# Optimization experiments

Hardware: AMD Instinct MI355X
Metric: run time of the kernel (lower is better)

Reference implementation:

```python
import jax, jax.numpy as jnp
import numpy as np

B, Q, H = 1, 1024, 2048
NH, NKV, HD = 32, 8, 64
KB = 2048
THETA = 10000.0
KB_MAX_TRAIN = 4096.0


def _bitlinear(x, w):
    """BitNet b1.58 linear: per-token int8 absmax activation quant + ternary weight quant (STE)."""
    a_scale = 127.0 / jnp.clip(jnp.max(jnp.abs(x), axis=-1, keepdims=True), 1e-5)
    xq = jnp.clip(jnp.round(x * a_scale), -128.0, 127.0) / a_scale
    w_scale = 1.0 / jnp.clip(jnp.mean(jnp.abs(w)), 1e-5)
    wq = jnp.clip(jnp.round(w * w_scale), -1.0, 1.0) / w_scale
    x_ste = x + jax.lax.stop_gradient(xq - x)
    w_ste = w + jax.lax.stop_gradient(wq - w)
    return jnp.einsum('bsh,oh->bso', x_ste, w_ste)


def _rope_cos_sin(position_ids):
    inv_freq = 1.0 / (THETA ** (jnp.arange(0, HD, 2, dtype=jnp.float32) / HD))  # [HD/2]
    freqs = position_ids.astype(jnp.float32)[..., None] * inv_freq  # [B,Q,HD/2]
    emb = jnp.concatenate([freqs, freqs], axis=-1)  # [B,Q,HD]
    return jnp.cos(emb)[:, None], jnp.sin(emb)[:, None]  # [B,1,Q,HD]


def _rotate_half(x):
    return jnp.concatenate([-x[..., HD // 2:], x[..., :HD // 2]], axis=-1)


def setup_inputs() -> dict:
    key = jax.random.key(0)
    ks = jax.random.split(key, 9)
    hidden_states = jax.random.normal(ks[0], (B, Q, H), jnp.float32)
    # additive causal mask
    attention_mask = jnp.triu(jnp.full((Q, Q), -1e9, jnp.float32), 1)[None, None]
    kb_keys = jax.random.normal(ks[1], (B, NH, KB, HD), jnp.float32)
    kb_values = jax.random.normal(ks[2], (B, NH, KB, HD), jnp.float32)
    s = 0.02
    Wq = jax.random.normal(ks[3], (NH * HD, H), jnp.float32) * s
    Wk = jax.random.normal(ks[4], (NKV * HD, H), jnp.float32) * s
    Wv = jax.random.normal(ks[5], (NKV * HD, H), jnp.float32) * s
    Wo = jax.random.normal(ks[6], (H, NH * HD), jnp.float32) * s
    Wq_new = jax.random.normal(ks[7], (NH * HD, H), jnp.float32) * s
    position_ids = jnp.arange(Q, dtype=jnp.int32)[None, :]
    return dict(hidden_states=hidden_states, attention_mask=attention_mask,
                kb_keys=kb_keys, kb_values=kb_values,
                Wq=Wq, Wk=Wk, Wv=Wv, Wo=Wo, Wq_new=Wq_new,
                position_ids=position_ids)


def reference(hidden_states, attention_mask, kb_keys, kb_values,
              Wq, Wk, Wv, Wo, Wq_new, position_ids):
    b, q_len, _ = hidden_states.shape
    # BitLinear QKV projections
    q = _bitlinear(hidden_states, Wq).reshape(b, q_len, NH, HD).transpose(0, 2, 1, 3)
    k = _bitlinear(hidden_states, Wk).reshape(b, q_len, NKV, HD).transpose(0, 2, 1, 3)
    v = _bitlinear(hidden_states, Wv).reshape(b, q_len, NKV, HD).transpose(0, 2, 1, 3)
    # RoPE on prompt q/k (KB query is NOT rotated, matching the source)
    cos, sin = _rope_cos_sin(position_ids)
    q = q * cos + _rotate_half(q) * sin
    k = k * cos + _rotate_half(k) * sin
    # GQA: repeat kv heads
    groups = NH // NKV
    k = jnp.repeat(k, groups, axis=1)
    v = jnp.repeat(v, groups, axis=1)
    # KB query via separate BitLinear
    kb_q = _bitlinear(hidden_states, Wq_new).reshape(b, q_len, NH, HD).transpose(0, 2, 1, 3)
    scale = 1.0 / jnp.sqrt(jnp.float32(HD))
    kb_len = kb_keys.shape[2]
    scores_kb = jnp.einsum('bhqd,bhkd->bhqk', kb_q, kb_keys) * scale
    scores_kb = scores_kb + (jnp.log(jnp.float32(KB_MAX_TRAIN)) - jnp.log(jnp.float32(kb_len)))
    scores_p = jnp.einsum('bhqd,bhkd->bhqk', q, k) * scale + attention_mask
    attn = jax.nn.softmax(jnp.concatenate([scores_kb, scores_p], axis=-1).astype(jnp.float32), axis=-1)
    out = (jnp.einsum('bhqk,bhkd->bhqd', attn[..., :kb_len], kb_values)
           + jnp.einsum('bhqk,bhkd->bhqd', attn[..., kb_len:], v))
    out = out.transpose(0, 2, 1, 3).reshape(b, q_len, NH * HD)
    return _bitlinear(out, Wo)
```

## Files before the change

kernel.cpp:

```cpp
#include <hip/hip_runtime.h>
#include <hip/hip_bf16.h>
#include <stdint.h>
#include <math.h>

#define cH    2048
#define cQ    1024
#define cNH   32
#define cNKV  8
#define cKB   2048

#define INV_BIG   (1.0f/4194304.0f)
#define INV_SMALL (1.0f/1048576.0f)

#define WS_SUMS 0
#define WS_DQ1  256
#define WS_DQ2  4352
#define WS_XQ   8448
#define WS_WALL 4202752
#define WS_QB   25174272
#define WS_KB   33562880
#define WS_VB   35660032
#define WS_QN   37757184
#define WS_ROPET 46145792


using short8  = __attribute__((ext_vector_type(8))) short;
using floatx4 = __attribute__((ext_vector_type(4))) float;

__device__ __forceinline__ void bsplit(float x, unsigned short& hi, unsigned short& lo) {
  __hip_bfloat16 h = __float2bfloat16(x);
  float hf = __bfloat162float(h);
  __hip_bfloat16 l = __float2bfloat16(x - hf);
  hi = *(unsigned short*)&h;
  lo = *(unsigned short*)&l;
}

__device__ __forceinline__ unsigned short tern(float v, float ws) {
  float q = rintf(v * ws);
  q = fminf(fmaxf(q, -1.0f), 1.0f);
  return (unsigned short)(__float_as_uint(q) >> 16);
}

__device__ __forceinline__ void gload16(const void* g, void* l) {
  __builtin_amdgcn_global_load_lds((const __attribute__((address_space(1))) void*)g,
                                   (__attribute__((address_space(3))) void*)l, 16, 0, 0);
}

__global__ void k_ropetab(const int* __restrict__ pos, float2* __restrict__ tab) {
  int i = blockIdx.x * 256 + threadIdx.x;
  int t = i >> 5, d = i & 31;
  double p = (double)pos[t];
  double ang = p * pow(10000.0, -(double)d / 32.0);
  tab[i] = make_float2((float)cos(ang), (float)sin(ang));
}

__global__ void k_abssum5(const float* __restrict__ w0, const float* __restrict__ w1,
                          const float* __restrict__ w2, const float* __restrict__ w3,
                          const float* __restrict__ w4, double* __restrict__ out) {
  __shared__ double red[256];
  const int seg = blockIdx.y;
  const float* w = seg == 0 ? w0 : seg == 1 ? w1 : seg == 2 ? w2 : seg == 3 ? w3 : w4;
  const int n4 = ((seg == 1 || seg == 2) ? 512 * 2048 : 2048 * 2048) / 4;
  double s = 0.0;
  for (int i = blockIdx.x * 256 + threadIdx.x; i < n4; i += gridDim.x * 256) {
    float4 x = *(const float4*)(w + (size_t)i * 4);
    s += (double)fabsf(x.x) + (double)fabsf(x.y) + (double)fabsf(x.z) + (double)fabsf(x.w);
  }
  red[threadIdx.x] = s;
  __syncthreads();
  for (int o = 128; o > 0; o >>= 1) {
    if ((int)threadIdx.x < o) red[threadIdx.x] += red[threadIdx.x + o];
    __syncthreads();
  }
  if (threadIdx.x == 0) atomicAdd(out + seg, red[0]);
}

__global__ void k_wquant4(const float* __restrict__ Wq, const float* __restrict__ Wk,
                          const float* __restrict__ Wv, const float* __restrict__ Wqn,
                          unsigned short* __restrict__ wall, const double* __restrict__ sums) {
  size_t i = ((size_t)blockIdx.x * 256 + threadIdx.x) * 4;
  const float* src; size_t off; double s; float inv;
  if (i < 4194304)      { src = Wq;  off = 0;       s = sums[0]; inv = INV_BIG; }
  else if (i < 5242880) { src = Wk;  off = 4194304; s = sums[1]; inv = INV_SMALL; }
  else if (i < 6291456) { src = Wv;  off = 5242880; s = sums[2]; inv = INV_SMALL; }
  else                  { src = Wqn; off = 6291456; s = sums[4]; inv = INV_BIG; }
  float ws = 1.0f / fmaxf((float)s * inv, 1e-5f);
  float4 x = *(const float4*)(src + (i - off));
  ushort4 o;
  o.x = tern(x.x, ws); o.y = tern(x.y, ws); o.z = tern(x.z, ws); o.w = tern(x.w, ws);
  *(ushort4*)(wall + i) = o;
}

__global__ void k_wquant(const float* __restrict__ w, unsigned short* __restrict__ wq,
                         const double* __restrict__ sum, float inv_n) {
  size_t i = ((size_t)blockIdx.x * 256 + threadIdx.x) * 4;
  float ws = 1.0f / fmaxf((float)(*sum) * inv_n, 1e-5f);
  float4 x = *(const float4*)(w + i);
  ushort4 o;
  o.x = tern(x.x, ws); o.y = tern(x.y, ws); o.z = tern(x.z, ws); o.w = tern(x.w, ws);
  *(ushort4*)(wq + i) = o;
}

__global__ void k_aquant(const float* __restrict__ x, unsigned short* __restrict__ xq,
                         float* __restrict__ dq, int K) {
  int t = blockIdx.x;
  const float4* xr = (const float4*)(x + (size_t)t * K);
  const int K4 = K / 4;
  __shared__ float red[256];
  float m = 0.0f;
  for (int i = threadIdx.x; i < K4; i += 256) {
    float4 v = xr[i];
    m = fmaxf(m, fmaxf(fmaxf(fabsf(v.x), fabsf(v.y)), fmaxf(fabsf(v.z), fabsf(v.w))));
  }
  red[threadIdx.x] = m;
  __syncthreads();
  for (int o = 128; o > 0; o >>= 1) {
    if ((int)threadIdx.x < o) red[threadIdx.x] = fmaxf(red[threadIdx.x], red[threadIdx.x + o]);
    __syncthreads();
  }
  float amax = fmaxf(red[0], 1e-5f);
  float as = 127.0f / amax;
  ushort4* xo = (ushort4*)(xq + (size_t)t * K);
  for (int i = threadIdx.x; i < K4; i += 256) {
    float4 v = xr[i];
    ushort4 o;
    float q;
    q = fminf(fmaxf(rintf(v.x * as), -128.0f), 127.0f); o.x = (unsigned short)(__float_as_uint(q) >> 16);
    q = fminf(fmaxf(rintf(v.y * as), -128.0f), 127.0f); o.y = (unsigned short)(__float_as_uint(q) >> 16);
    q = fminf(fmaxf(rintf(v.z * as), -128.0f), 127.0f); o.z = (unsigned short)(__float_as_uint(q) >> 16);
    q = fminf(fmaxf(rintf(v.w * as), -128.0f), 127.0f); o.w = (unsigned short)(__float_as_uint(q) >> 16);
    xo[i] = o;
  }
  if (threadIdx.x == 0) dq[t] = amax / 127.0f;
}

__global__ __launch_bounds__(256) void k_gemm_mfma(
    const unsigned short* __restrict__ Aq, const unsigned short* __restrict__ Ball,
    const float* __restrict__ adq, const double* __restrict__ sums,
    const float2* __restrict__ ropetab,
    float* __restrict__ oQ, unsigned short* __restrict__ oKhi,
    unsigned short* __restrict__ oKlo,
    float* __restrict__ oV, float* __restrict__ oQN, int mode) {
  __shared__ __attribute__((aligned(16))) unsigned short As[2][128 * 64];
  __shared__ __attribute__((aligned(16))) unsigned short Bs[2][128 * 64];
  const int t = threadIdx.x;
  const int lane = t & 63;
  const int row16 = lane & 15, q = lane >> 4;
  const int w = t >> 6;
  const int wm = (w >> 1) * 64, wn = (w & 1) * 64;
  const int bx = blockIdx.x;
  const int m0 = blockIdx.y * 128;
  const unsigned short* Bp = Ball + (size_t)bx * 128 * 2048;
  const int swr = row16 & 7;

  floatx4 acc[4][4];
#pragma unroll
  for (int g = 0; g < 4; ++g)
#pragma unroll
    for (int h = 0; h < 4; ++h) acc[g][h] = (floatx4){0.f, 0.f, 0.f, 0.f};

  auto stageAB = [&](int k0s, int b) {
#pragma unroll
    for (int i = 0; i < 4; ++i) {
      int c = t + 256 * i;
      int row = c >> 3, g8 = c & 7;
      int sa = (g8 ^ (row & 7)) * 8;
      gload16(Aq + (size_t)(m0 + row) * 2048 + k0s + sa, &As[b][w * 512 + i * 2048]);
      gload16(Bp + (size_t)row * 2048 + k0s + sa, &Bs[b][w * 512 + i * 2048]);
    }
  };

  stageAB(0, 0);
  for (int k0 = 0; k0 < 2048; k0 += 64) {
    const int cur = (k0 >> 6) & 1;
    const int kn = (k0 + 64 < 2048) ? k0 + 64 : k0;
    stageAB(kn, cur ^ 1);
    asm volatile("s_waitcnt vmcnt(8)" ::: "memory");
    __builtin_amdgcn_s_barrier();
#pragma unroll
    for (int kk = 0; kk < 2; ++kk) {
      short8 af[4], bf[4];
      const int sw = ((kk * 4 + q) ^ swr) << 3;
#pragma unroll
      for (int g = 0; g < 4; ++g)
        af[g] = *(const short8*)&As[cur][(wm + g * 16 + row16) * 64 + sw];
#pragma unroll
      for (int h = 0; h < 4; ++h)
        bf[h] = *(const short8*)&Bs[cur][(wn + h * 16 + row16) * 64 + sw];
#pragma unroll
      for (int g = 0; g < 4; ++g)
#pragma unroll
        for (int h = 0; h < 4; ++h)
          acc[g][h] = __builtin_amdgcn_mfma_f32_16x16x32_bf16(af[g], bf[h], acc[g][h], 0, 0, 0);
    }
    __builtin_amdgcn_s_barrier();
  }
  asm volatile("s_waitcnt vmcnt(0)" ::: "memory");

  float* outp = nullptr; int Nout = 0, nb0; float wdq;
  if (mode == 1)      { outp = oQ;  Nout = 2048; nb0 = bx * 128;        wdq = fmaxf((float)sums[3] * INV_BIG,   1e-5f); }
  else if (bx < 16)   { outp = oQ;  Nout = 2048; nb0 = bx * 128;        wdq = fmaxf((float)sums[0] * INV_BIG,   1e-5f); }
  else if (bx < 20)   {             Nout = 512;  nb0 = (bx - 16) * 128; wdq = fmaxf((float)sums[1] * INV_SMALL, 1e-5f); }
  else if (bx < 24)   { outp = oV;  Nout = 512;  nb0 = (bx - 20) * 128; wdq = fmaxf((float)sums[2] * INV_SMALL, 1e-5f); }
  else                { outp = oQN; Nout = 2048; nb0 = (bx - 24) * 128; wdq = fmaxf((float)sums[4] * INV_BIG,   1e-5f); }

  if (mode == 0 && bx < 20) {
#pragma unroll
    for (int g = 0; g < 4; ++g)
#pragma unroll
      for (int r = 0; r < 4; ++r) {
        int m = m0 + wm + g * 16 + q * 4 + r;
        float s = adq[m] * wdq;
        float2 cs0 = ropetab[m * 32 + row16];
        float2 cs1 = ropetab[m * 32 + 16 + row16];
        float v0 = acc[g][0][r] * s, v1 = acc[g][1][r] * s;
        float v2 = acc[g][2][r] * s, v3 = acc[g][3][r] * s;
        float o0 = v0 * cs0.x - v2 * cs0.y;
        float o2 = v2 * cs0.x + v0 * cs0.y;
        float o1 = v1 * cs1.x - v3 * cs1.y;
        float o3 = v3 * cs1.x + v1 * cs1.y;
        if (bx < 16) {
          size_t base = (size_t)m * Nout + nb0 + wn;
          outp[base + row16]      = o0;
          outp[base + 16 + row16] = o1;
          outp[base + 32 + row16] = o2;
          outp[base + 48 + row16] = o3;
        } else {
          int hkv_ = (nb0 + wn) >> 6;
          int kt_ = m >> 6, rr = m & 63;
          size_t tb = ((size_t)(hkv_ * 16 + kt_)) * 4096;
          int lbase = (rr & 15) + ((row16 >> 3) << 4);
          int ntb = (rr >> 4) * 512 + (row16 & 7);
          unsigned short hi, lo; int ix;
          bsplit(o0, hi, lo); ix = ntb + (lbase     ) * 8;          oKhi[tb + ix] = hi; oKlo[tb + ix] = lo;
          bsplit(o1, hi, lo); ix = ntb + (lbase + 32) * 8;          oKhi[tb + ix] = hi; oKlo[tb + ix] = lo;
          bsplit(o2, hi, lo); ix = ntb + (lbase     ) * 8 + 2048;   oKhi[tb + ix] = hi; oKlo[tb + ix] = lo;
          bsplit(o3, hi, lo); ix = ntb + (lbase + 32) * 8 + 2048;   oKhi[tb + ix] = hi; oKlo[tb + ix] = lo;
        }
      }
  } else {
#pragma unroll
    for (int g = 0; g < 4; ++g)
#pragma unroll
      for (int r = 0; r < 4; ++r) {
        int m = m0 + wm + g * 16 + q * 4 + r;
        float s = adq[m] * wdq;
#pragma unroll
        for (int h = 0; h < 4; ++h)
          outp[(size_t)m * Nout + nb0 + wn + h * 16 + row16] = acc[g][h][r] * s;
      }
  }
}

__global__ __launch_bounds__(256) void k_gemm64(
    const unsigned short* __restrict__ Aq, const unsigned short* __restrict__ Bq,
    const float* __restrict__ adq, const double* __restrict__ sums,
    float* __restrict__ out) {
  __shared__ __attribute__((aligned(16))) unsigned short As[2][64 * 64];
  __shared__ __attribute__((aligned(16))) unsigned short Bs[2][64 * 64];
  const int t = threadIdx.x;
  const int lane = t & 63;
  const int row16 = lane & 15, q = lane >> 4;
  const int w = t >> 6;
  const int wm = (w >> 1) * 32, wn = (w & 1) * 32;
  const int nb0 = blockIdx.x * 64;
  const int m0 = blockIdx.y * 64;
  const int swr = row16 & 7;

  floatx4 acc[2][2];
#pragma unroll
  for (int g = 0; g < 2; ++g)
#pragma unroll
    for (int h = 0; h < 2; ++h) acc[g][h] = (floatx4){0.f, 0.f, 0.f, 0.f};

  auto stageAB = [&](int k0s, int b) {
#pragma unroll
    for (int i = 0; i < 2; ++i) {
      int c = t + 256 * i;
      int row = c >> 3, g8 = c & 7;
      int sa = (g8 ^ (row & 7)) * 8;
      gload16(Aq + (size_t)(m0 + row) * 2048 + k0s + sa, &As[b][w * 512 + i * 2048]);
      gload16(Bq + (size_t)(nb0 + row) * 2048 + k0s + sa, &Bs[b][w * 512 + i * 2048]);
    }
  };

  stageAB(0, 0);
  for (int k0 = 0; k0 < 2048; k0 += 64) {
    const int cur = (k0 >> 6) & 1;
    const int kn = (k0 + 64 < 2048) ? k0 + 64 : k0;
    stageAB(kn, cur ^ 1);
    asm volatile("s_waitcnt vmcnt(4)" ::: "memory");
    __builtin_amdgcn_s_barrier();
#pragma unroll
    for (int kk = 0; kk < 2; ++kk) {
      short8 af[2], bf[2];
      const int sw = ((kk * 4 + q) ^ swr) << 3;
#pragma unroll
      for (int g = 0; g < 2; ++g)
        af[g] = *(const short8*)&As[cur][(wm + g * 16 + row16) * 64 + sw];
#pragma unroll
      for (int h = 0; h < 2; ++h)
        bf[h] = *(const short8*)&Bs[cur][(wn + h * 16 + row16) * 64 + sw];
#pragma unroll
      for (int g = 0; g < 2; ++g)
#pragma unroll
        for (int h = 0; h < 2; ++h)
          acc[g][h] = __builtin_amdgcn_mfma_f32_16x16x32_bf16(af[g], bf[h], acc[g][h], 0, 0, 0);
    }
    __builtin_amdgcn_s_barrier();
  }
  asm volatile("s_waitcnt vmcnt(0)" ::: "memory");

  float wdq = fmaxf((float)sums[3] * INV_BIG, 1e-5f);
#pragma unroll
  for (int g = 0; g < 2; ++g)
#pragma unroll
    for (int r = 0; r < 4; ++r) {
      int m = m0 + wm + g * 16 + q * 4 + r;
      float s = adq[m] * wdq;
#pragma unroll
      for (int h = 0; h < 2; ++h)
        out[(size_t)m * 2048 + nb0 + wn + h * 16 + row16] = acc[g][h][r] * s;
    }
}

__global__ __launch_bounds__(256) void k_prep(
    const float* __restrict__ kbv, const float* __restrict__ Vb,
    unsigned short* __restrict__ vtKBhi, unsigned short* __restrict__ vtPhi,
    float* __restrict__ kbk) {
  const int b = blockIdx.x;
  const int t = threadIdx.x;
  if (b >= 1152) {
    float* tile = kbk + (size_t)(b - 1152) * 4096;
    float v[2][8];
#pragma unroll
    for (int u = 0; u < 2; ++u) {
      int task = t + 256 * u;
      int r = task >> 3, s = task & 7;
      *(float4*)&v[u][0] = *(const float4*)(tile + r * 64 + s * 8);
      *(float4*)&v[u][4] = *(const float4*)(tile + r * 64 + s * 8 + 4);
    }
    __syncthreads();
    unsigned short* up = (unsigned short*)tile;
#pragma unroll
    for (int u = 0; u < 2; ++u) {
      int task = t + 256 * u;
      int r = task >> 3, s = task & 7;
      union { unsigned short u16[8]; uint4 q; } hi, lo;
#pragma unroll
      for (int j = 0; j < 8; ++j) bsplit(v[u][j], hi.u16[j], lo.u16[j]);
      size_t off = (size_t)(((s >> 2) * 4 + (r >> 4)) * 512 + ((r & 15) + ((s & 3) << 4)) * 8);
      *(uint4*)(up + off)        = hi.q;
      *(uint4*)(up + 4096 + off) = lo.q;
    }
    return;
  }
  __shared__ float Lf[64 * 65];
  const float* src; unsigned short *dhi, *dlo; int srcStride;
  if (b < 1024) {
    int h = b >> 5, kt = b & 31;
    src = kbv + ((size_t)h * cKB + kt * 64) * 64; srcStride = 64;
    dhi = vtKBhi + (size_t)b * 4096; dlo = dhi + 4194304;
  } else {
    int bb = b - 1024;
    int hkv = bb >> 4, kt = bb & 15;
    src = Vb + (size_t)(kt * 64) * 512 + hkv * 64; srcStride = 512;
    dhi = vtPhi + (size_t)bb * 4096; dlo = dhi + 524288;
  }
#pragma unroll
  for (int i = 0; i < 4; ++i) {
    int c = t + 256 * i;
    int row = c >> 4, c4 = (c & 15) * 4;
    float4 x = *(const float4*)(src + (size_t)row * srcStride + c4);
    Lf[row * 65 + c4 + 0] = x.x;
    Lf[row * 65 + c4 + 1] = x.y;
    Lf[row * 65 + c4 + 2] = x.z;
    Lf[row * 65 + c4 + 3] = x.w;
  }
  __syncthreads();
#pragma unroll
  for (int u = 0; u < 2; ++u) {
    int task = t + 256 * u;
    int d = task >> 3, s = task & 7;
    union { unsigned short u16[8]; uint4 q; } hi, lo;
#pragma unroll
    for (int j = 0; j < 8; ++j) bsplit(Lf[(s * 8 + j) * 65 + d], hi.u16[j], lo.u16[j]);
    size_t off = (size_t)(((s >> 2) * 4 + (d >> 4)) * 512 + ((d & 15) + ((s & 3) << 4)) * 8);
    *(uint4*)(dhi + off) = hi.q;
    *(uint4*)(dlo + off) = lo.q;
  }
}

__global__ __launch_bounds__(256, 2) void k_attn_mfma(
    const float* __restrict__ Qr, float* qnctx,
    const unsigned short* __restrict__ KPhi,
    const unsigned short* __restrict__ kbkS,
    const unsigned short* __restrict__ vtKBhi,
    const unsigned short* __restrict__ vtPhi) {
  __shared__ __attribute__((aligned(16))) unsigned int Pbuf[4][16 * 68];

  const int t = threadIdx.x;
  const int lane = t & 63;
  const int col = lane & 15;
  const int quad = lane >> 4;
  const int w = t >> 6;
  const int h = blockIdx.x;
  const int q0 = blockIdx.y * 64;
  const int hkv = h >> 2;
  const float kbbias = 0.69314718055994531f;
  unsigned int* Pw = &Pbuf[w][0];
  const int fl = lane * 8;

  short8 qAh[2], qAl[2];
  short8 qBh[2], qBl[2];
  {
#pragma unroll
    for (int kk = 0; kk < 2; ++kk) {
      const size_t off = (size_t)(q0 + w * 16 + col) * 2048 + h * 64 + kk * 32 + quad * 8;
      float4 a = *(const float4*)(qnctx + off);
      float4 b = *(const float4*)(qnctx + off + 4);
      float xs[8] = {a.x, a.y, a.z, a.w, b.x, b.y, b.z, b.w};
#pragma unroll
      for (int j = 0; j < 8; ++j) {
        unsigned short hi, lo;
        bsplit(xs[j] * 0.125f, hi, lo);
        qAh[kk][j] = (short)hi; qAl[kk][j] = (short)lo;
      }
      float4 c = *(const float4*)(Qr + off);
      float4 d = *(const float4*)(Qr + off + 4);
      float ys[8] = {c.x, c.y, c.z, c.w, d.x, d.y, d.z, d.w};
#pragma unroll
      for (int j = 0; j < 8; ++j) {
        unsigned short hi, lo;
        bsplit(ys[j] * 0.125f, hi, lo);
        qBh[kk][j] = (short)hi; qBl[kk][j] = (short)lo;
      }
    }
  }

  floatx4 acco[4];
  float m_[4], l_[4];
#pragma unroll
  for (int nt = 0; nt < 4; ++nt) acco[nt] = (floatx4){0.f, 0.f, 0.f, 0.f};
#pragma unroll
  for (int r = 0; r < 4; ++r) { m_[r] = -3.0e38f; l_[r] = 0.f; }

  const int ntiles = 32 + (q0 >> 6) + 1;

  short8 kh[2][4], kl[2][4];
  short8 vh[2][4], vl[2][4];

  auto loadK = [&](int kt2) {
    const unsigned short *ph, *pl;
    if (kt2 < 32) { const size_t tk = (size_t)(h * 32 + kt2);
                    ph = kbkS + tk * 8192; pl = ph + 4096; }
    else          { const size_t tk = (size_t)(hkv * 16 + (kt2 - 32));
                    ph = KPhi + tk * 4096; pl = ph + 524288; }
#pragma unroll
    for (int kk = 0; kk < 2; ++kk)
#pragma unroll
      for (int nt = 0; nt < 4; ++nt) {
        kh[kk][nt] = *(const short8*)(ph + (kk * 4 + nt) * 512 + fl);
        kl[kk][nt] = *(const short8*)(pl + (kk * 4 + nt) * 512 + fl);
      }
  };
  auto loadV = [&](int kt2) {
    const unsigned short *ph, *pl;
    if (kt2 < 32) { const size_t tk = (size_t)(h * 32 + kt2);
                    ph = vtKBhi + tk * 4096; pl = ph + 4194304; }
    else          { const size_t tk = (size_t)(hkv * 16 + (kt2 - 32));
                    ph = vtPhi + tk * 4096; pl = ph + 524288; }
#pragma unroll
    for (int kk = 0; kk < 2; ++kk)
#pragma unroll
      for (int nt = 0; nt < 4; ++nt) {
        vh[kk][nt] = *(const short8*)(ph + (kk * 4 + nt) * 512 + fl);
        vl[kk][nt] = *(const short8*)(pl + (kk * 4 + nt) * 512 + fl);
      }
  };

  loadK(0);

  for (int kt = 0; kt < ntiles; ++kt) {
    const bool isKB = kt < 32;
    loadV(kt);
    __builtin_amdgcn_s_barrier();

    floatx4 accs[4];
#pragma unroll
    for (int nt = 0; nt < 4; ++nt) accs[nt] = (floatx4){0.f, 0.f, 0.f, 0.f};
    if (isKB) {
#pragma unroll
      for (int kk = 0; kk < 2; ++kk)
#pragma unroll
        for (int nt = 0; nt < 4; ++nt) {
          accs[nt] = __builtin_amdgcn_mfma_f32_16x16x32_bf16(qAh[kk], kh[kk][nt], accs[nt], 0, 0, 0);
          accs[nt] = __builtin_amdgcn_mfma_f32_16x16x32_bf16(qAl[kk], kh[kk][nt], accs[nt], 0, 0, 0);
          accs[nt] = __builtin_amdgcn_mfma_f32_16x16x32_bf16(qAh[kk], kl[kk][nt], accs[nt], 0, 0, 0);
        }
    } else {
#pragma unroll
      for (int kk = 0; kk < 2; ++kk)
#pragma unroll
        for (int nt = 0; nt < 4; ++nt) {
          accs[nt] = __builtin_amdgcn_mfma_f32_16x16x32_bf16(qBh[kk], kh[kk][nt], accs[nt], 0, 0, 0);
          accs[nt] = __builtin_amdgcn_mfma_f32_16x16x32_bf16(qBl[kk], kh[kk][nt], accs[nt], 0, 0, 0);
          accs[nt] = __builtin_amdgcn_mfma_f32_16x16x32_bf16(qBh[kk], kl[kk][nt], accs[nt], 0, 0, 0);
        }
    }

    float sv[4][4];
    if (isKB) {
#pragma unroll
      for (int nt = 0; nt < 4; ++nt)
#pragma unroll
        for (int r = 0; r < 4; ++r) sv[nt][r] = accs[nt][r] + kbbias;
    } else if (kt < ntiles - 1) {
#pragma unroll
      for (int nt = 0; nt < 4; ++nt)
#pragma unroll
        for (int r = 0; r < 4; ++r) sv[nt][r] = accs[nt][r];
    } else {
#pragma unroll
      for (int nt = 0; nt < 4; ++nt) {
        int kl_ = nt * 16 + col;
#pragma unroll
        for (int r = 0; r < 4; ++r) {
          int ql_ = w * 16 + quad * 4 + r;
          sv[nt][r] = accs[nt][r] + ((kl_ <= ql_) ? 0.0f : -1e9f);
        }
      }
    }
#pragma unroll
    for (int r = 0; r < 4; ++r) {
      float rmax = fmaxf(fmaxf(sv[0][r], sv[1][r]), fmaxf(sv[2][r], sv[3][r]));
#pragma unroll
      for (int off = 8; off; off >>= 1) rmax = fmaxf(rmax, __shfl_xor(rmax, off));
      float mnew = fmaxf(m_[r], rmax);
      float alpha = __expf(m_[r] - mnew);
      float psum = 0.f;
#pragma unroll
      for (int nt = 0; nt < 4; ++nt) {
        float p = __expf(sv[nt][r] - mnew);
        sv[nt][r] = p;
        psum += p;
      }
#pragma unroll
      for (int off = 8; off; off >>= 1) psum += __shfl_xor(psum, off);
      l_[r] = l_[r] * alpha + psum;
      m_[r] = mnew;
#pragma unroll
      for (int nt = 0; nt < 4; ++nt) acco[nt][r] *= alpha;
    }

    loadK(kt + 1 < ntiles ? kt + 1 : kt);

#pragma unroll
    for (int nt = 0; nt < 4; ++nt)
#pragma unroll
      for (int r = 0; r < 4; ++r) {
        unsigned xb = __float_as_uint(sv[nt][r]);
        float hf = __uint_as_float(xb & 0xffff0000u);
        unsigned db = __float_as_uint(sv[nt][r] - hf);
        Pw[(quad * 4 + r) * 68 + nt * 16 + col] = (xb >> 16) | (db & 0xffff0000u);
      }

#pragma unroll
    for (int kk = 0; kk < 2; ++kk) {
      uint4 pa = *(const uint4*)&Pw[col * 68 + kk * 32 + quad * 8];
      uint4 pb = *(const uint4*)&Pw[col * 68 + kk * 32 + quad * 8 + 4];
      union { unsigned int u[4]; short8 s; } uh, ul;
      uh.u[0] = (pa.x & 0xffffu) | (pa.y << 16);
      uh.u[1] = (pa.z & 0xffffu) | (pa.w << 16);
      uh.u[2] = (pb.x & 0xffffu) | (pb.y << 16);
      uh.u[3] = (pb.z & 0xffffu) | (pb.w << 16);
      ul.u[0] = (pa.x >> 16) | (pa.y & 0xffff0000u);
      ul.u[1] = (pa.z >> 16) | (pa.w & 0xffff0000u);
      ul.u[2] = (pb.x >> 16) | (pb.y & 0xffff0000u);
      ul.u[3] = (pb.z >> 16) | (pb.w & 0xffff0000u);
      short8 ph8 = uh.s, pl8 = ul.s;
#pragma unroll
      for (int nt = 0; nt < 4; ++nt) {
        acco[nt] = __builtin_amdgcn_mfma_f32_16x16x32_bf16(ph8, vh[kk][nt], acco[nt], 0, 0, 0);
        acco[nt] = __builtin_amdgcn_mfma_f32_16x16x32_bf16(pl8, vh[kk][nt], acco[nt], 0, 0, 0);
        acco[nt] = __builtin_amdgcn_mfma_f32_16x16x32_bf16(ph8, vl[kk][nt], acco[nt], 0, 0, 0);
      }
    }
  }

#pragma unroll
  for (int r = 0; r < 4; ++r) {
    float linv = 1.0f / l_[r];
#pragma unroll
    for (int nt = 0; nt < 4; ++nt)
      qnctx[(size_t)(q0 + w * 16 + quad * 4 + r) * 2048 + h * 64 + nt * 16 + col] =
          acco[nt][r] * linv;
  }
}

extern "C" void kernel_launch(void* const* d_in, const int* in_sizes, int n_in,
                              void* d_out, int out_size, void* d_ws, size_t ws_size,
                              hipStream_t stream) {
  (void)in_sizes; (void)n_in; (void)out_size; (void)ws_size;
  const float* hidden = (const float*)d_in[0];
  float* kbk = (float*)d_in[2];
  const float* kbv = (const float*)d_in[3];
  const float* Wq  = (const float*)d_in[4];
  const float* Wk  = (const float*)d_in[5];
  const float* Wv  = (const float*)d_in[6];
  const float* Wo  = (const float*)d_in[7];
  const float* Wqn = (const float*)d_in[8];
  const int*   pos = (const int*)d_in[9];

  char* ws = (char*)d_ws;
  double* sums = (double*)(ws + WS_SUMS);
  float* dq1 = (float*)(ws + WS_DQ1);
  float* dq2 = (float*)(ws + WS_DQ2);
  unsigned short* xq   = (unsigned short*)(ws + WS_XQ);
  unsigned short* wall = (unsigned short*)(ws + WS_WALL);
  unsigned short* vtKBhi = (unsigned short*)(ws + WS_WALL);
  unsigned short* vtPhi  = (unsigned short*)(ws + WS_WALL + 16777216);
  unsigned short* wqo  = (unsigned short*)(ws + WS_QB);
  float* Qb  = (float*)(ws + WS_QB);
  unsigned short* KPhi = (unsigned short*)(ws + WS_KB);
  unsigned short* KPlo = KPhi + 524288;
  float* Vb  = (float*)(ws + WS_VB);
  float* QNC = (float*)(ws + WS_QN);
  float2* ropetab = (float2*)(ws + WS_ROPET);

  hipMemsetAsync(sums, 0, 64, stream);

  k_ropetab<<<128, 256, 0, stream>>>(pos, ropetab);
  k_abssum5<<<dim3(128, 5), 256, 0, stream>>>(Wq, Wk, Wv, Wo, Wqn, sums);
  k_wquant4<<<10240, 256, 0, stream>>>(Wq, Wk, Wv, Wqn, wall, sums);
  k_aquant<<<cQ, 256, 0, stream>>>(hidden, xq, dq1, cH);

  k_gemm_mfma<<<dim3(40, 8), 256, 0, stream>>>(xq, wall, dq1, sums, ropetab,
                                               Qb, KPhi, KPlo, Vb, QNC, 0);

  k_prep<<<1152 + 1024, 256, 0, stream>>>(kbv, Vb, vtKBhi, vtPhi, kbk);

  k_attn_mfma<<<dim3(cNH, cQ / 64), 256, 0, stream>>>(
      Qb, QNC, KPhi, (const unsigned short*)kbk, vtKBhi, vtPhi);

  k_wquant<<<4096, 256, 0, stream>>>(Wo, wqo, sums + 3, INV_BIG);
  k_aquant<<<cQ, 256, 0, stream>>>(QNC, xq, dq2, cH);

  k_gemm64<<<dim3(32, 16), 256, 0, stream>>>(xq, wqo, dq2, sums, (float*)d_out);
}
```

Before: 371.8 us.

## Process two 16-row query groups per wave in attention to reuse K/V fragments

Result: slower. 417.5 us (+12.3%).

```diff
diff --git a/kernel.cpp b/kernel.cpp
--- a/kernel.cpp
+++ b/kernel.cpp
@@ -391,13 +391,13 @@
   }
 }
 
-__global__ __launch_bounds__(256, 2) void k_attn_mfma(
+__global__ __launch_bounds__(128, 1) void k_attn_mfma(
     const float* __restrict__ Qr, float* qnctx,
     const unsigned short* __restrict__ KPhi,
     const unsigned short* __restrict__ kbkS,
     const unsigned short* __restrict__ vtKBhi,
     const unsigned short* __restrict__ vtPhi) {
-  __shared__ __attribute__((aligned(16))) unsigned int Pbuf[4][16 * 68];
+  __shared__ __attribute__((aligned(16))) unsigned int Pbuf[2][32 * 68];
 
   const int t = threadIdx.x;
   const int lane = t & 63;
@@ -411,12 +411,13 @@
   unsigned int* Pw = &Pbuf[w][0];
   const int fl = lane * 8;
 
-  short8 qAh[2], qAl[2];
-  short8 qBh[2], qBl[2];
-  {
+  short8 qAh[2][2], qAl[2][2];
+  short8 qBh[2][2], qBl[2][2];
+#pragma unroll
+  for (int g = 0; g < 2; ++g)
 #pragma unroll
     for (int kk = 0; kk < 2; ++kk) {
-      const size_t off = (size_t)(q0 + w * 16 + col) * 2048 + h * 64 + kk * 32 + quad * 8;
+      const size_t off = (size_t)(q0 + w * 32 + g * 16 + col) * 2048 + h * 64 + kk * 32 + quad * 8;
       float4 a = *(const float4*)(qnctx + off);
       float4 b = *(const float4*)(qnctx + off + 4);
       float xs[8] = {a.x, a.y, a.z, a.w, b.x, b.y, b.z, b.w};
@@ -424,7 +425,7 @@
       for (int j = 0; j < 8; ++j) {
         unsigned short hi, lo;
         bsplit(xs[j] * 0.125f, hi, lo);
-        qAh[kk][j] = (short)hi; qAl[kk][j] = (short)lo;
+        qAh[g][kk][j] = (short)hi; qAl[g][kk][j] = (short)lo;
       }
       float4 c = *(const float4*)(Qr + off);
       float4 d = *(const float4*)(Qr + off + 4);
@@ -433,17 +434,20 @@
       for (int j = 0; j < 8; ++j) {
         unsigned short hi, lo;
         bsplit(ys[j] * 0.125f, hi, lo);
-        qBh[kk][j] = (short)hi; qBl[kk][j] = (short)lo;
-      }
-    }
-  }
-
-  floatx4 acco[4];
-  float m_[4], l_[4];
-#pragma unroll
-  for (int nt = 0; nt < 4; ++nt) acco[nt] = (floatx4){0.f, 0.f, 0.f, 0.f};
-#pragma unroll
-  for (int r = 0; r < 4; ++r) { m_[r] = -3.0e38f; l_[r] = 0.f; }
+        qBh[g][kk][j] = (short)hi; qBl[g][kk][j] = (short)lo;
+      }
+    }
+
+  floatx4 acco[2][4];
+  float m_[2][4], l_[2][4];
+#pragma unroll
+  for (int g = 0; g < 2; ++g)
+#pragma unroll
+    for (int nt = 0; nt < 4; ++nt) acco[g][nt] = (floatx4){0.f, 0.f, 0.f, 0.f};
+#pragma unroll
+  for (int g = 0; g < 2; ++g)
+#pragma unroll
+    for (int r = 0; r < 4; ++r) { m_[g][r] = -3.0e38f; l_[g][r] = 0.f; }
 
   const int ntiles = 32 + (q0 >> 6) + 1;
 
@@ -486,116 +490,136 @@
     loadV(kt);
     __builtin_amdgcn_s_barrier();
 
-    floatx4 accs[4];
-#pragma unroll
-    for (int nt = 0; nt < 4; ++nt) accs[nt] = (floatx4){0.f, 0.f, 0.f, 0.f};
+    floatx4 accs[2][4];
+#pragma unroll
+    for (int g = 0; g < 2; ++g)
+#pragma unroll
+      for (int nt = 0; nt < 4; ++nt) accs[g][nt] = (floatx4){0.f, 0.f, 0.f, 0.f};
     if (isKB) {
 #pragma unroll
-      for (int kk = 0; kk < 2; ++kk)
+      for (int g = 0; g < 2; ++g)
+#pragma unroll
+        for (int kk = 0; kk < 2; ++kk)
+#pragma unroll
+          for (int nt = 0; nt < 4; ++nt) {
+            accs[g][nt] = __builtin_amdgcn_mfma_f32_16x16x32_bf16(qAh[g][kk], kh[kk][nt], accs[g][nt], 0, 0, 0);
+            accs[g][nt] = __builtin_amdgcn_mfma_f32_16x16x32_bf16(qAl[g][kk], kh[kk][nt], accs[g][nt], 0, 0, 0);
+            accs[g][nt] = __builtin_amdgcn_mfma_f32_16x16x32_bf16(qAh[g][kk], kl[kk][nt], accs[g][nt], 0, 0, 0);
+          }
+    } else {
+#pragma unroll
+      for (int g = 0; g < 2; ++g)
+#pragma unroll
+        for (int kk = 0; kk < 2; ++kk)
+#pragma unroll
+          for (int nt = 0; nt < 4; ++nt) {
+            accs[g][nt] = __builtin_amdgcn_mfma_f32_16x16x32_bf16(qBh[g][kk], kh[kk][nt], accs[g][nt], 0, 0, 0);
+            accs[g][nt] = __builtin_amdgcn_mfma_f32_16x16x32_bf16(qBl[g][kk], kh[kk][nt], accs[g][nt], 0, 0, 0);
+            accs[g][nt] = __builtin_amdgcn_mfma_f32_16x16x32_bf16(qBh[g][kk], kl[kk][nt], accs[g][nt], 0, 0, 0);
+          }
+    }
+
+    float sv[2][4][4];
+    if (isKB) {
+#pragma unroll
+      for (int g = 0; g < 2; ++g)
+#pragma unroll
+        for (int nt = 0; nt < 4; ++nt)
+#pragma unroll
+          for (int r = 0; r < 4; ++r) sv[g][nt][r] = accs[g][nt][r] + kbbias;
+    } else if (kt < ntiles - 1) {
+#pragma unroll
+      for (int g = 0; g < 2; ++g)
+#pragma unroll
+        for (int nt = 0; nt < 4; ++nt)
+#pragma unroll
+          for (int r = 0; r < 4; ++r) sv[g][nt][r] = accs[g][nt][r];
+    } else {
+#pragma unroll
+      for (int g = 0; g < 2; ++g)
 #pragma unroll
         for (int nt = 0; nt < 4; ++nt) {
-          accs[nt] = __builtin_amdgcn_mfma_f32_16x16x32_bf16(qAh[kk], kh[kk][nt], accs[nt], 0, 0, 0);
-          accs[nt] = __builtin_amdgcn_mfma_f32_16x16x32_bf16(qAl[kk], kh[kk][nt], accs[nt], 0, 0, 0);
-          accs[nt] = __builtin_amdgcn_mfma_f32_16x16x32_bf16(qAh[kk], kl[kk][nt], accs[nt], 0, 0, 0);
+          int kl_ = nt * 16 + col;
+#pragma unroll
+          for (int r = 0; r < 4; ++r) {
+            int ql_ = w * 32 + g * 16 + quad * 4 + r;
+            sv[g][nt][r] = accs[g][nt][r] + ((kl_ <= ql_) ? 0.0f : -1e9f);
+          }
         }
-    } else {
-#pragma unroll
-      for (int kk = 0; kk < 2; ++kk)
+    }
+#pragma unroll
+    for (int g = 0; g < 2; ++g)
+#pragma unroll
+      for (int r = 0; r < 4; ++r) {
+        float rmax = fmaxf(fmaxf(sv[g][0][r], sv[g][1][r]), fmaxf(sv[g][2][r], sv[g][3][r]));
+#pragma unroll
+        for (int off = 8; off; off >>= 1) rmax = fmaxf(rmax, __shfl_xor(rmax, off));
+        float mnew = fmaxf(m_[g][r], rmax);
+        float alpha = __expf(m_[g][r] - mnew);
+        float psum = 0.f;
 #pragma unroll
         for (int nt = 0; nt < 4; ++nt) {
-          accs[nt] = __builtin_amdgcn_mfma_f32_16x16x32_bf16(qBh[kk], kh[kk][nt], accs[nt], 0, 0, 0);
-          accs[nt] = __builtin_amdgcn_mfma_f32_16x16x32_bf16(qBl[kk], kh[kk][nt], accs[nt], 0, 0, 0);
-          accs[nt] = __builtin_amdgcn_mfma_f32_16x16x32_bf16(qBh[kk], kl[kk][nt], accs[nt], 0, 0, 0);
+          float p = __expf(sv[g][nt][r] - mnew);
+          sv[g][nt][r] = p;
+          psum += p;
         }
-    }
-
-    float sv[4][4];
-    if (isKB) {
+#pragma unroll
+        for (int off = 8; off; off >>= 1) psum += __shfl_xor(psum, off);
+        l_[g][r] = l_[g][r] * alpha + psum;
+        m_[g][r] = mnew;
+#pragma unroll
+        for (int nt = 0; nt < 4; ++nt) acco[g][nt][r] *= alpha;
+      }
+
+    loadK(kt + 1 < ntiles ? kt + 1 : kt);
+
+#pragma unroll
+    for (int g = 0; g < 2; ++g)
 #pragma unroll
       for (int nt = 0; nt < 4; ++nt)
 #pragma unroll
-        for (int r = 0; r < 4; ++r) sv[nt][r] = accs[nt][r] + kbbias;
-    } else if (kt < ntiles - 1) {
+        for (int r = 0; r < 4; ++r) {
+          unsigned xb = __float_as_uint(sv[g][nt][r]);
+          float hf = __uint_as_float(xb & 0xffff0000u);
+          unsigned db = __float_as_uint(sv[g][nt][r] - hf);
+          Pw[(g * 16 + quad * 4 + r) * 68 + nt * 16 + col] = (xb >> 16) | (db & 0xffff0000u);
+        }
+
+#pragma unroll
+    for (int kk = 0; kk < 2; ++kk)
+#pragma unroll
+      for (int g = 0; g < 2; ++g) {
+        uint4 pa = *(const uint4*)&Pw[(g * 16 + col) * 68 + kk * 32 + quad * 8];
+        uint4 pb = *(const uint4*)&Pw[(g * 16 + col) * 68 + kk * 32 + quad * 8 + 4];
+        union { unsigned int u[4]; short8 s; } uh, ul;
+        uh.u[0] = (pa.x & 0xffffu) | (pa.y << 16);
+        uh.u[1] = (pa.z & 0xffffu) | (pa.w << 16);
+        uh.u[2] = (pb.x & 0xffffu) | (pb.y << 16);
+        uh.u[3] = (pb.z & 0xffffu) | (pb.w << 16);
+        ul.u[0] = (pa.x >> 16) | (pa.y & 0xffff0000u);
+        ul.u[1] = (pa.z >> 16) | (pa.w & 0xffff0000u);
+        ul.u[2] = (pb.x >> 16) | (pb.y & 0xffff0000u);
+        ul.u[3] = (pb.z >> 16) | (pb.w & 0xffff0000u);
+        short8 ph8 = uh.s, pl8 = ul.s;
+#pragma unroll
+        for (int nt = 0; nt < 4; ++nt) {
+          acco[g][nt] = __builtin_amdgcn_mfma_f32_16x16x32_bf16(ph8, vh[kk][nt], acco[g][nt], 0, 0, 0);
+          acco[g][nt] = __builtin_amdgcn_mfma_f32_16x16x32_bf16(pl8, vh[kk][nt], acco[g][nt], 0, 0, 0);
+          acco[g][nt] = __builtin_amdgcn_mfma_f32_16x16x32_bf16(ph8, vl[kk][nt], acco[g][nt], 0, 0, 0);
+        }
+      }
+  }
+
+#pragma unroll
+  for (int g = 0; g < 2; ++g)
+#pragma unroll
+    for (int r = 0; r < 4; ++r) {
+      float linv = 1.0f / l_[g][r];
 #pragma unroll
       for (int nt = 0; nt < 4; ++nt)
-#pragma unroll
-        for (int r = 0; r < 4; ++r) sv[nt][r] = accs[nt][r];
-    } else {
-#pragma unroll
-      for (int nt = 0; nt < 4; ++nt) {
-        int kl_ = nt * 16 + col;
-#pragma unroll
-        for (int r = 0; r < 4; ++r) {
-          int ql_ = w * 16 + quad * 4 + r;
-          sv[nt][r] = accs[nt][r] + ((kl_ <= ql_) ? 0.0f : -1e9f);
-        }
-      }
-    }
-#pragma unroll
-    for (int r = 0; r < 4; ++r) {
-      float rmax = fmaxf(fmaxf(sv[0][r], sv[1][r]), fmaxf(sv[2][r], sv[3][r]));
-#pragma unroll
-      for (int off = 8; off; off >>= 1) rmax = fmaxf(rmax, __shfl_xor(rmax, off));
-      float mnew = fmaxf(m_[r], rmax);
-      float alpha = __expf(m_[r] - mnew);
-      float psum = 0.f;
-#pragma unroll
-      for (int nt = 0; nt < 4; ++nt) {
-        float p = __expf(sv[nt][r] - mnew);
-        sv[nt][r] = p;
-        psum += p;
-      }
-#pragma unroll
-      for (int off = 8; off; off >>= 1) psum += __shfl_xor(psum, off);
-      l_[r] = l_[r] * alpha + psum;
-      m_[r] = mnew;
-#pragma unroll
-      for (int nt = 0; nt < 4; ++nt) acco[nt][r] *= alpha;
-    }
-
-    loadK(kt + 1 < ntiles ? kt + 1 : kt);
-
-#pragma unroll
-    for (int nt = 0; nt < 4; ++nt)
-#pragma unroll
-      for (int r = 0; r < 4; ++r) {
-        unsigned xb = __float_as_uint(sv[nt][r]);
-        float hf = __uint_as_float(xb & 0xffff0000u);
-        unsigned db = __float_as_uint(sv[nt][r] - hf);
-        Pw[(quad * 4 + r) * 68 + nt * 16 + col] = (xb >> 16) | (db & 0xffff0000u);
-      }
-
-#pragma unroll
-    for (int kk = 0; kk < 2; ++kk) {
-      uint4 pa = *(const uint4*)&Pw[col * 68 + kk * 32 + quad * 8];
-      uint4 pb = *(const uint4*)&Pw[col * 68 + kk * 32 + quad * 8 + 4];
-      union { unsigned int u[4]; short8 s; } uh, ul;
-      uh.u[0] = (pa.x & 0xffffu) | (pa.y << 16);
-      uh.u[1] = (pa.z & 0xffffu) | (pa.w << 16);
-      uh.u[2] = (pb.x & 0xffffu) | (pb.y << 16);
-      uh.u[3] = (pb.z & 0xffffu) | (pb.w << 16);
-      ul.u[0] = (pa.x >> 16) | (pa.y & 0xffff0000u);
-      ul.u[1] = (pa.z >> 16) | (pa.w & 0xffff0000u);
-      ul.u[2] = (pb.x >> 16) | (pb.y & 0xffff0000u);
-      ul.u[3] = (pb.z >> 16) | (pb.w & 0xffff0000u);
-      short8 ph8 = uh.s, pl8 = ul.s;
-#pragma unroll
-      for (int nt = 0; nt < 4; ++nt) {
-        acco[nt] = __builtin_amdgcn_mfma_f32_16x16x32_bf16(ph8, vh[kk][nt], acco[nt], 0, 0, 0);
-        acco[nt] = __builtin_amdgcn_mfma_f32_16x16x32_bf16(pl8, vh[kk][nt], acco[nt], 0, 0, 0);
-        acco[nt] = __builtin_amdgcn_mfma_f32_16x16x32_bf16(ph8, vl[kk][nt], acco[nt], 0, 0, 0);
-      }
-    }
-  }
-
-#pragma unroll
-  for (int r = 0; r < 4; ++r) {
-    float linv = 1.0f / l_[r];
-#pragma unroll
-    for (int nt = 0; nt < 4; ++nt)
-      qnctx[(size_t)(q0 + w * 16 + quad * 4 + r) * 2048 + h * 64 + nt * 16 + col] =
-          acco[nt][r] * linv;
-  }
+        qnctx[(size_t)(q0 + w * 32 + g * 16 + quad * 4 + r) * 2048 + h * 64 + nt * 16 + col] =
+            acco[g][nt][r] * linv;
+    }
 }
 
 extern "C" void kernel_launch(void* const* d_in, const int* in_sizes, int n_in,
@@ -640,7 +664,7 @@
 
   k_prep<<<1152 + 1024, 256, 0, stream>>>(kbv, Vb, vtKBhi, vtPhi, kbk);
 
-  k_attn_mfma<<<dim3(cNH, cQ / 64), 256, 0, stream>>>(
+  k_attn_mfma<<<dim3(cNH, cQ / 64), 128, 0, stream>>>(
       Qb, QNC, KPhi, (const unsigned short*)kbk, vtKBhi, vtPhi);
 
   k_wquant<<<4096, 256, 0, stream>>>(Wo, wqo, sums + 3, INV_BIG);
```

## Split PV matmul across waves by output column slice sharing P in LDS

Applied to the files above, without the earlier changes.

After: 391.0 us. +5.1%, slower.

```diff
diff --git a/kernel.cpp b/kernel.cpp
--- a/kernel.cpp
+++ b/kernel.cpp
@@ -397,7 +397,8 @@
     const unsigned short* __restrict__ kbkS,
     const unsigned short* __restrict__ vtKBhi,
     const unsigned short* __restrict__ vtPhi) {
-  __shared__ __attribute__((aligned(16))) unsigned int Pbuf[4][16 * 68];
+  __shared__ __attribute__((aligned(16))) unsigned int Pbuf[64 * 68];
+  __shared__ __attribute__((aligned(16))) float aex[64];
 
   const int t = threadIdx.x;
   const int lane = t & 63;
@@ -408,7 +409,6 @@
   const int q0 = blockIdx.y * 64;
   const int hkv = h >> 2;
   const float kbbias = 0.69314718055994531f;
-  unsigned int* Pw = &Pbuf[w][0];
   const int fl = lane * 8;
 
   short8 qAh[2], qAl[2];
@@ -441,14 +441,14 @@
   floatx4 acco[4];
   float m_[4], l_[4];
 #pragma unroll
-  for (int nt = 0; nt < 4; ++nt) acco[nt] = (floatx4){0.f, 0.f, 0.f, 0.f};
+  for (int g = 0; g < 4; ++g) acco[g] = (floatx4){0.f, 0.f, 0.f, 0.f};
 #pragma unroll
   for (int r = 0; r < 4; ++r) { m_[r] = -3.0e38f; l_[r] = 0.f; }
 
   const int ntiles = 32 + (q0 >> 6) + 1;
 
   short8 kh[2][4], kl[2][4];
-  short8 vh[2][4], vl[2][4];
+  short8 vh[2], vl[2];
 
   auto loadK = [&](int kt2) {
     const unsigned short *ph, *pl;
@@ -471,12 +471,10 @@
     else          { const size_t tk = (size_t)(hkv * 16 + (kt2 - 32));
                     ph = vtPhi + tk * 4096; pl = ph + 524288; }
 #pragma unroll
-    for (int kk = 0; kk < 2; ++kk)
-#pragma unroll
-      for (int nt = 0; nt < 4; ++nt) {
-        vh[kk][nt] = *(const short8*)(ph + (kk * 4 + nt) * 512 + fl);
-        vl[kk][nt] = *(const short8*)(pl + (kk * 4 + nt) * 512 + fl);
-      }
+    for (int kk = 0; kk < 2; ++kk) {
+      vh[kk] = *(const short8*)(ph + (kk * 4 + w) * 512 + fl);
+      vl[kk] = *(const short8*)(pl + (kk * 4 + w) * 512 + fl);
+    }
   };
 
   loadK(0);
@@ -531,6 +529,7 @@
         }
       }
     }
+    float alpha_[4];
 #pragma unroll
     for (int r = 0; r < 4; ++r) {
       float rmax = fmaxf(fmaxf(sv[0][r], sv[1][r]), fmaxf(sv[2][r], sv[3][r]));
@@ -549,8 +548,7 @@
       for (int off = 8; off; off >>= 1) psum += __shfl_xor(psum, off);
       l_[r] = l_[r] * alpha + psum;
       m_[r] = mnew;
-#pragma unroll
-      for (int nt = 0; nt < 4; ++nt) acco[nt][r] *= alpha;
+      alpha_[r] = alpha;
     }
 
     loadK(kt + 1 < ntiles ? kt + 1 : kt);
@@ -562,39 +560,51 @@
         unsigned xb = __float_as_uint(sv[nt][r]);
         float hf = __uint_as_float(xb & 0xffff0000u);
         unsigned db = __float_as_uint(sv[nt][r] - hf);
-        Pw[(quad * 4 + r) * 68 + nt * 16 + col] = (xb >> 16) | (db & 0xffff0000u);
-      }
-
-#pragma unroll
-    for (int kk = 0; kk < 2; ++kk) {
-      uint4 pa = *(const uint4*)&Pw[col * 68 + kk * 32 + quad * 8];
-      uint4 pb = *(const uint4*)&Pw[col * 68 + kk * 32 + quad * 8 + 4];
-      union { unsigned int u[4]; short8 s; } uh, ul;
-      uh.u[0] = (pa.x & 0xffffu) | (pa.y << 16);
-      uh.u[1] = (pa.z & 0xffffu) | (pa.w << 16);
-      uh.u[2] = (pb.x & 0xffffu) | (pb.y << 16);
-      uh.u[3] = (pb.z & 0xffffu) | (pb.w << 16);
-      ul.u[0] = (pa.x >> 16) | (pa.y & 0xffff0000u);
-      ul.u[1] = (pa.z >> 16) | (pa.w & 0xffff0000u);
-      ul.u[2] = (pb.x >> 16) | (pb.y & 0xffff0000u);
-      ul.u[3] = (pb.z >> 16) | (pb.w & 0xffff0000u);
-      short8 ph8 = uh.s, pl8 = ul.s;
-#pragma unroll
-      for (int nt = 0; nt < 4; ++nt) {
-        acco[nt] = __builtin_amdgcn_mfma_f32_16x16x32_bf16(ph8, vh[kk][nt], acco[nt], 0, 0, 0);
-        acco[nt] = __builtin_amdgcn_mfma_f32_16x16x32_bf16(pl8, vh[kk][nt], acco[nt], 0, 0, 0);
-        acco[nt] = __builtin_amdgcn_mfma_f32_16x16x32_bf16(ph8, vl[kk][nt], acco[nt], 0, 0, 0);
-      }
-    }
-  }
-
-#pragma unroll
-  for (int r = 0; r < 4; ++r) {
-    float linv = 1.0f / l_[r];
-#pragma unroll
-    for (int nt = 0; nt < 4; ++nt)
-      qnctx[(size_t)(q0 + w * 16 + quad * 4 + r) * 2048 + h * 64 + nt * 16 + col] =
-          acco[nt][r] * linv;
+        Pbuf[(w * 16 + quad * 4 + r) * 68 + nt * 16 + col] = (xb >> 16) | (db & 0xffff0000u);
+      }
+    if (col < 4) aex[w * 16 + quad * 4 + col] = alpha_[col];
+
+    asm volatile("s_waitcnt lgkmcnt(0)" ::: "memory");
+    __builtin_amdgcn_s_barrier();
+
+#pragma unroll
+    for (int g = 0; g < 4; ++g) {
+      float4 ar = *(const float4*)&aex[g * 16 + quad * 4];
+      acco[g][0] *= ar.x; acco[g][1] *= ar.y; acco[g][2] *= ar.z; acco[g][3] *= ar.w;
+    }
+#pragma unroll
+    for (int kk = 0; kk < 2; ++kk)
+#pragma unroll
+      for (int g = 0; g < 4; ++g) {
+        uint4 pa = *(const uint4*)&Pbuf[(g * 16 + col) * 68 + kk * 32 + quad * 8];
+        uint4 pb = *(const uint4*)&Pbuf[(g * 16 + col) * 68 + kk * 32 + quad * 8 + 4];
+        union { unsigned int u[4]; short8 s; } uh, ul;
+        uh.u[0] = (pa.x & 0xffffu) | (pa.y << 16);
+        uh.u[1] = (pa.z & 0xffffu) | (pa.w << 16);
+        uh.u[2] = (pb.x & 0xffffu) | (pb.y << 16);
+        uh.u[3] = (pb.z & 0xffffu) | (pb.w << 16);
+        ul.u[0] = (pa.x >> 16) | (pa.y & 0xffff0000u);
+        ul.u[1] = (pa.z >> 16) | (pa.w & 0xffff0000u);
+        ul.u[2] = (pb.x >> 16) | (pb.y & 0xffff0000u);
+        ul.u[3] = (pb.z >> 16) | (pb.w & 0xffff0000u);
+        short8 ph8 = uh.s, pl8 = ul.s;
+        acco[g] = __builtin_amdgcn_mfma_f32_16x16x32_bf16(ph8, vh[kk], acco[g], 0, 0, 0);
+        acco[g] = __builtin_amdgcn_mfma_f32_16x16x32_bf16(pl8, vh[kk], acco[g], 0, 0, 0);
+        acco[g] = __builtin_amdgcn_mfma_f32_16x16x32_bf16(ph8, vl[kk], acco[g], 0, 0, 0);
+      }
+  }
+
+  __syncthreads();
+  if (col < 4) aex[w * 16 + quad * 4 + col] = l_[col];
+  __syncthreads();
+#pragma unroll
+  for (int g = 0; g < 4; ++g) {
+    float4 lr = *(const float4*)&aex[g * 16 + quad * 4];
+    float4 li = {1.0f / lr.x, 1.0f / lr.y, 1.0f / lr.z, 1.0f / lr.w};
+#pragma unroll
+    for (int r = 0; r < 4; ++r)
+      qnctx[(size_t)(q0 + g * 16 + quad * 4 + r) * 2048 + h * 64 + w * 16 + col] =
+          acco[g][r] * ((const float*)&li)[r];
   }
 }
 
```
